# Kernel optimization log

Hardware: AMD Instinct MI355X
Metric: run time of the kernel (lower is better)

The kernel has to match this reference:

```python
import jax, jax.numpy as jnp
import numpy as np

B, C, H, W, G = 4, 256, 64, 64, 4
K = 9  # 3x3 kernel


def _conv1x1(x, w, b):
    return jnp.einsum('bchw,oc->bohw', x, w) + b[None, :, None, None]


def _deform_conv(V, offset, mask, weight, groups):
    # torchvision modulated deform_conv2d, stride=1, pad=1, dil=1, no bias.
    Bs, Cc, Hh, Ww = V.shape
    Cg = Cc // groups
    # offset layout: [B, og, K, 2(y,x), H, W]
    off = offset.reshape(Bs, groups, K, 2, Hh, Ww)
    ky, kx = jnp.meshgrid(jnp.arange(3), jnp.arange(3), indexing='ij')
    ky = ky.reshape(K).astype(offset.dtype)
    kx = kx.reshape(K).astype(offset.dtype)
    hh = jnp.arange(Hh, dtype=offset.dtype)
    ww = jnp.arange(Ww, dtype=offset.dtype)
    # sampling positions [B, G, K, H, W]
    py = off[:, :, :, 0] + (hh[:, None] - 1.0)[None, None, None] + ky[None, None, :, None, None]
    px = off[:, :, :, 1] + (ww[None, :] - 1.0)[None, None, None] + kx[None, None, :, None, None]
    y0f = jnp.floor(py)
    x0f = jnp.floor(px)
    fy = py - y0f
    fx = px - x0f
    y0 = y0f.astype(jnp.int32)
    x0 = x0f.astype(jnp.int32)
    Vg = V.reshape(Bs, groups, Cg, Hh * Ww)

    def gather(yi, xi, wgt):
        valid = (yi >= 0) & (yi < Hh) & (xi >= 0) & (xi < Ww)
        idx = (jnp.clip(yi, 0, Hh - 1) * Ww + jnp.clip(xi, 0, Ww - 1)).reshape(Bs, groups, 1, K * Hh * Ww)
        vals = jnp.take_along_axis(Vg, jnp.broadcast_to(idx, (Bs, groups, Cg, K * Hh * Ww)), axis=3)
        vals = vals.reshape(Bs, groups, Cg, K, Hh, Ww)
        return vals * (wgt * valid.astype(wgt.dtype))[:, :, None]

    sampled = (gather(y0, x0, (1.0 - fy) * (1.0 - fx))
               + gather(y0, x0 + 1, (1.0 - fy) * fx)
               + gather(y0 + 1, x0, fy * (1.0 - fx))
               + gather(y0 + 1, x0 + 1, fy * fx))  # [B, G, Cg, K, H, W]
    m = mask.reshape(Bs, groups, K, Hh, Ww)
    wk = weight.reshape(groups, Cc // groups, Cg, K)
    out = jnp.einsum('bgikhw,bgkhw,goik->bgohw', sampled, m, wk)
    return out.reshape(Bs, Cc, Hh, Ww)


def setup_inputs() -> dict:
    key = jax.random.key(0)
    ks = jax.random.split(key, 12)
    inp = {
        'rife_feat': jax.random.normal(ks[0], (B, C, H, W), jnp.float32),
        'd0': jax.random.normal(ks[1], (B, C, H, W), jnp.float32),
        'd1': jax.random.normal(ks[2], (B, C, H, W), jnp.float32),
        'wq': jax.random.normal(ks[3], (C, C), jnp.float32) * (1.0 / np.sqrt(C)),
        'bq': jax.random.normal(ks[4], (C,), jnp.float32) * 0.01,
        'wk': jax.random.normal(ks[5], (C, C), jnp.float32) * (1.0 / np.sqrt(C)),
        'bk': jax.random.normal(ks[6], (C,), jnp.float32) * 0.01,
        'wv': jax.random.normal(ks[7], (C, C), jnp.float32) * (1.0 / np.sqrt(C)),
        'bv': jax.random.normal(ks[8], (C,), jnp.float32) * 0.01,
        'w_off': jax.random.normal(ks[9], (27 * G, 2 * C, 3, 3), jnp.float32) * 0.02,
        'b_off': jnp.zeros((27 * G,), jnp.float32),
        'dcn_w': jax.random.normal(ks[10], (C, C // G, 3, 3), jnp.float32) * 0.05,
        'gamma': jnp.ones((1,), jnp.float32),
    }
    return inp


def reference(rife_feat, d0, d1, wq, bq, wk, bk, wv, bv, w_off, b_off, dcn_w, gamma):
    Qs = jnp.concatenate([rife_feat, rife_feat], axis=0)  # [2B, C, H, W]
    Ds = jnp.concatenate([d0, d1], axis=0)
    Q = _conv1x1(Qs, wq, bq)
    Kf = _conv1x1(Ds, wk, bk)
    V = _conv1x1(Ds, wv, bv)
    comb = jnp.concatenate([Q, Kf], axis=1)  # [2B, 2C, H, W]
    out = jax.lax.conv_general_dilated(comb, w_off, (1, 1), [(1, 1), (1, 1)],
                                       dimension_numbers=('NCHW', 'OIHW', 'NCHW'))
    out = out + b_off[None, :, None, None]  # [2B, 27G, H, W]
    n = out.shape[1] // 3
    o1, o2, mlog = out[:, :n], out[:, n:2 * n], out[:, 2 * n:]
    offset = jnp.concatenate([o1, o2], axis=1)  # [2B, 18G, H, W]
    mask = jax.nn.sigmoid(mlog)
    aligned = _deform_conv(V, offset, mask, dcn_w, G)
    a0, a1 = aligned[:B], aligned[B:]
    fused = rife_feat + gamma * (a0 + a1)
    return fused, offset[:B], offset[B:]
```

## Files before the change

### kernel.cpp

```cpp
#include <hip/hip_runtime.h>
#include <math.h>

#define HW   4096
#define CDIM 256

typedef float f32x4  __attribute__((ext_vector_type(4)));
typedef short short8 __attribute__((ext_vector_type(8)));

#define FUSED_SZ (4ULL*256*HW)
#define OFF_SZ   (4ULL*72*HW)

static __device__ __forceinline__ unsigned short f2b(float f) {
    unsigned u = __float_as_uint(f);
    unsigned r = (u + 0x7fffu + ((u >> 16) & 1u)) >> 16;
    return (unsigned short)r;
}
static __device__ __forceinline__ float b2f(short h) {
    return __uint_as_float(((unsigned)(unsigned short)h) << 16);
}
static __device__ __forceinline__ unsigned pk_bf16(float a, float b) {
    unsigned r;
    asm("v_cvt_pk_bf16_f32 %0, %1, %2" : "=v"(r) : "v"(a), "v"(b));
    return r;
}
union U8 { unsigned u[4]; short8 s; };

__global__ __launch_bounds__(256) void wprep(const float* __restrict__ w_off,
                                             unsigned short* __restrict__ wT2)
{
    int idx = blockIdx.x * 256 + threadIdx.x;
    if (idx >= 9 * 128 * 512) return;
    int kk  = idx / (128 * 512);
    int rem = idx - kk * 128 * 512;
    int o = rem >> 9;
    int c = rem & 511;
    float v = (o < 108) ? w_off[((size_t)o * 512 + c) * 9 + kk] : 0.f;
    size_t flat = ((size_t)(kk * 16 + (c >> 5)) * 128 + o) * 32 + (c & 31);
    wT2[flat] = f2b(v);
}

__global__ __launch_bounds__(256) void dprep(const float* __restrict__ dcn_w,
                                             unsigned short* __restrict__ dcnwT)
{
    int idx = blockIdx.x * 256 + threadIdx.x;
    if (idx >= 9 * 256 * 64) return;
    int k   = idx / (256 * 64);
    int rem = idx - k * 256 * 64;
    int og = rem >> 6;
    int i  = rem & 63;
    int g = og >> 6, ol = og & 63;
    size_t flat = ((size_t)((k * 4 + g) * 2 + (i >> 5)) * 64 + ol) * 32 + (i & 31);
    dcnwT[flat] = f2b(dcn_w[((size_t)og * 64 + i) * 9 + k]);
}

__global__ __launch_bounds__(256) void qwprep(
    const float* __restrict__ wq, const float* __restrict__ wk,
    const float* __restrict__ wv, unsigned short* __restrict__ wqkvT)
{
    int idx = blockIdx.x * 256 + threadIdx.x;
    int o = idx >> 8;
    int c = idx & 255;
    float v = (o < 256) ? wq[(size_t)o * 256 + c]
            : (o < 512) ? wk[(size_t)(o - 256) * 256 + c]
                        : wv[(size_t)(o - 512) * 256 + c];
    wqkvT[idx] = f2b(v);
}

__global__ __launch_bounds__(256) void xprep(
    const float* __restrict__ rife, const float* __restrict__ d0,
    const float* __restrict__ d1, unsigned short* __restrict__ xT)
{
    const int pix0 = blockIdx.x * 64;
    const int img  = blockIdx.y;
    const int t    = threadIdx.x;

    const float* src = (img < 4) ? rife + (size_t)img * CDIM * HW
                     : (img < 8) ? d0 + (size_t)(img - 4) * CDIM * HW
                                 : d1 + (size_t)(img - 8) * CDIM * HW;
    unsigned short* dst = xT + (size_t)img * 4096 * 256;

    __shared__ float tile[64][65];

    for (int c0 = 0; c0 < 256; c0 += 64) {
        #pragma unroll
        for (int r = 0; r < 16; ++r) {
            int idx = t + r * 256;
            int c = idx >> 6, pp = idx & 63;
            tile[c][pp] = src[(size_t)(c0 + c) * HW + pix0 + pp];
        }
        __syncthreads();
        const int pix = t >> 2, cq = t & 3;
        const int cb = cq * 16;
        uint4 p0, p1;
        p0.x = (unsigned)f2b(tile[cb+0][pix])  | ((unsigned)f2b(tile[cb+1][pix])  << 16);
        p0.y = (unsigned)f2b(tile[cb+2][pix])  | ((unsigned)f2b(tile[cb+3][pix])  << 16);
        p0.z = (unsigned)f2b(tile[cb+4][pix])  | ((unsigned)f2b(tile[cb+5][pix])  << 16);
        p0.w = (unsigned)f2b(tile[cb+6][pix])  | ((unsigned)f2b(tile[cb+7][pix])  << 16);
        p1.x = (unsigned)f2b(tile[cb+8][pix])  | ((unsigned)f2b(tile[cb+9][pix])  << 16);
        p1.y = (unsigned)f2b(tile[cb+10][pix]) | ((unsigned)f2b(tile[cb+11][pix]) << 16);
        p1.z = (unsigned)f2b(tile[cb+12][pix]) | ((unsigned)f2b(tile[cb+13][pix]) << 16);
        p1.w = (unsigned)f2b(tile[cb+14][pix]) | ((unsigned)f2b(tile[cb+15][pix]) << 16);
        unsigned short* p = dst + (size_t)(pix0 + pix) * 256 + c0 + cb;
        *(uint4*)p = p0;
        *(uint4*)(p + 8) = p1;
        __syncthreads();
    }
}

__global__ __launch_bounds__(256) void qkv_mfma(
    const unsigned short* __restrict__ xT,
    const unsigned short* __restrict__ wqkvT,
    const float* __restrict__ bq, const float* __restrict__ bk,
    const float* __restrict__ bv,
    unsigned short* __restrict__ comb_t, unsigned short* __restrict__ vbuf_t)
{
    const int pix0 = blockIdx.x * 64;
    const int type = blockIdx.y;
    const int s    = blockIdx.z;
    const int t    = threadIdx.x;
    const int wvi  = t >> 6;
    const int lane = t & 63;
    const int q    = lane >> 4;
    const int rl   = lane & 15;

    const int img = (type == 0) ? (s & 3) : (4 + s);
    const short8* X = (const short8*)(xT + (size_t)img * 4096 * 256);
    const short8* W = (const short8*)(wqkvT + (size_t)(type * 256 + wvi * 64) * 256);
    const float* bias = (type == 0) ? bq : (type == 1) ? bk : bv;

    f32x4 acc[4][4];
    #pragma unroll
    for (int mf = 0; mf < 4; ++mf)
        #pragma unroll
        for (int nf = 0; nf < 4; ++nf)
            acc[mf][nf] = (f32x4){0.f, 0.f, 0.f, 0.f};

    #pragma unroll
    for (int c8 = 0; c8 < 32; c8 += 4) {
        short8 a[4], b[4];
        #pragma unroll
        for (int mf = 0; mf < 4; ++mf)
            a[mf] = W[(size_t)(mf * 16 + rl) * 32 + c8 + q];
        #pragma unroll
        for (int nf = 0; nf < 4; ++nf)
            b[nf] = X[(size_t)(pix0 + nf * 16 + rl) * 32 + c8 + q];
        #pragma unroll
        for (int mf = 0; mf < 4; ++mf)
            #pragma unroll
            for (int nf = 0; nf < 4; ++nf)
                acc[mf][nf] = __builtin_amdgcn_mfma_f32_16x16x32_bf16(a[mf], b[nf], acc[mf][nf], 0, 0, 0);
    }

    const int CH = (type < 2) ? 512 : 256;
    unsigned short* dst = (type < 2)
        ? comb_t + (size_t)s * 4096 * 512 + type * 256
        : vbuf_t + (size_t)s * 4096 * 256;
    #pragma unroll
    for (int mf = 0; mf < 4; ++mf) {
        const int o_loc = wvi * 64 + mf * 16 + q * 4;
        const float4 bz = *(const float4*)(bias + o_loc);
        #pragma unroll
        for (int nf = 0; nf < 4; ++nf) {
            const int pix = pix0 + nf * 16 + rl;
            uint2 pk;
            pk.x = pk_bf16(acc[mf][nf][0] + bz.x, acc[mf][nf][1] + bz.y);
            pk.y = pk_bf16(acc[mf][nf][2] + bz.z, acc[mf][nf][3] + bz.w);
            *(uint2*)(dst + (size_t)pix * CH + o_loc) = pk;
        }
    }
}

__global__ __launch_bounds__(256) void offconv_mfma(
    const unsigned short* __restrict__ comb_t,
    const unsigned short* __restrict__ wT2,
    const float* __restrict__ b_off,
    float* __restrict__ dout, float* __restrict__ mask_ws)
{
    const int bid = blockIdx.x;
    const int s = bid & 7;
    const int h = bid >> 3;
    const int t = threadIdx.x;
    const int lane = t & 63;
    const int wid  = t >> 6;
    const int q    = lane >> 4;
    const int rl   = lane & 15;

    __shared__ __align__(16) unsigned short tb[2][792 * 8];

    const short8* cbv = (const short8*)comb_t + (size_t)s * 4096 * 64;
    const short8* wv  = (const short8*)wT2;

    const int i1 = t + 256, i2 = t + 512, i3 = t + 768;

    auto sload = [&](int idx, int c8) -> short8 {
        int x = idx >> 2, cq = idx & 3;
        int ky = x / 66, xx = x - ky * 66;
        int hh = h + ky - 1, gx = xx - 1;
        short8 v = {0, 0, 0, 0, 0, 0, 0, 0};
        if (hh >= 0 && hh < 64 && gx >= 0 && gx < 64)
            v = cbv[(size_t)(hh * 64 + gx) * 64 + c8 + cq];
        return v;
    };
    auto swrite = [&](unsigned short* buf, int idx, short8 v) {
        int x = idx >> 2, cq = idx & 3;
        int qs = cq ^ ((x >> 1) & 3);
        *((short8*)buf + x * 4 + qs) = v;
    };

    f32x4 acc[2][4];
    #pragma unroll
    for (int ma = 0; ma < 2; ++ma)
        #pragma unroll
        for (int nf = 0; nf < 4; ++nf)
            acc[ma][nf] = (f32x4){0.f, 0.f, 0.f, 0.f};

    short8 r0 = sload(t, 0), r1 = sload(i1, 0), r2 = sload(i2, 0);
    short8 r3 = {0,0,0,0,0,0,0,0};
    if (i3 < 792) r3 = sload(i3, 0);
    swrite(tb[0], t, r0); swrite(tb[0], i1, r1); swrite(tb[0], i2, r2);
    if (i3 < 792) swrite(tb[0], i3, r3);
    __syncthreads();

    for (int sl = 0; sl < 16; ++sl) {
        const int c8 = sl * 4;
        if (sl < 15) {
            r0 = sload(t, c8 + 4); r1 = sload(i1, c8 + 4); r2 = sload(i2, c8 + 4);
            if (i3 < 792) r3 = sload(i3, c8 + 4);
        }
        short8 a[2][9];
        #pragma unroll
        for (int ma = 0; ma < 2; ++ma) {
            const int o = (wid * 2 + ma) * 16 + rl;
            #pragma unroll
            for (int kk = 0; kk < 9; ++kk)
                a[ma][kk] = wv[((size_t)(kk * 16 + sl) * 128 + o) * 4 + q];
        }
        const unsigned short* bufc = tb[sl & 1];
        #pragma unroll
        for (int kk = 0; kk < 9; ++kk) {
            const int ky = kk / 3, kx = kk % 3;
            #pragma unroll
            for (int nf = 0; nf < 4; ++nf) {
                const int xr = ky * 66 + nf * 16 + rl + kx;
                short8 b = *((const short8*)bufc + xr * 4 + (q ^ ((xr >> 1) & 3)));
                acc[0][nf] = __builtin_amdgcn_mfma_f32_16x16x32_bf16(a[0][kk], b, acc[0][nf], 0, 0, 0);
                acc[1][nf] = __builtin_amdgcn_mfma_f32_16x16x32_bf16(a[1][kk], b, acc[1][nf], 0, 0, 0);
            }
        }
        if (sl < 15) {
            unsigned short* bufn = tb[(sl + 1) & 1];
            swrite(bufn, t, r0); swrite(bufn, i1, r1); swrite(bufn, i2, r2);
            if (i3 < 792) swrite(bufn, i3, r3);
        }
        __syncthreads();
    }

    const size_t obase = FUSED_SZ + (s < 4 ? 0 : OFF_SZ) + (size_t)(s & 3) * 72 * HW + (size_t)h * 64;
    const size_t mbase = (size_t)s * 36 * HW + (size_t)h * 64;
    #pragma unroll
    for (int ma = 0; ma < 2; ++ma) {
        #pragma unroll
        for (int r = 0; r < 4; ++r) {
            const int o = (wid * 2 + ma) * 16 + q * 4 + r;
            if (o >= 108) continue;
            const float bz = b_off[o];
            #pragma unroll
            for (int nf = 0; nf < 4; ++nf) {
                const int w = nf * 16 + rl;
                float v = acc[ma][nf][r] + bz;
                if (o < 72)
                    dout[obase + (size_t)o * HW + w] = v;
                else
                    mask_ws[mbase + (size_t)(o - 72) * HW + w] = 1.f / (1.f + expf(-v));
            }
        }
    }
}

__global__ __launch_bounds__(256) void dcn_fuse_mfma(
    const float* __restrict__ rife, const unsigned short* __restrict__ dcnwT,
    const float* __restrict__ gamma,
    const unsigned short* __restrict__ vbuf_t, const float* __restrict__ mask_ws,
    float* __restrict__ dout)
{
    const int bid = blockIdx.x;
    const int c   = bid & 15;
    const int h   = bid >> 4;
    const int b   = c >> 2;
    const int g   = c & 3;
    const int t    = threadIdx.x;
    const int wv   = t >> 6;
    const int lane = t & 63;
    const int q    = lane >> 4;
    const int rl   = lane & 15;
    const int pix  = wv * 16 + rl;

    const short8* aT = (const short8*)dcnwT;

    f32x4 acc[4];
    #pragma unroll
    for (int ma = 0; ma < 4; ++ma) acc[ma] = (f32x4){0.f, 0.f, 0.f, 0.f};

    const size_t obA = FUSED_SZ + (size_t)b * 72 * HW + (size_t)(g * 18) * HW + (size_t)h * 64 + pix;
    const size_t obB = obA + OFF_SZ;
    const size_t mbA = (size_t)b * 36 * HW + (size_t)(g * 9) * HW + (size_t)h * 64 + pix;
    const size_t mbB = mbA + 4ULL * 36 * HW;

    auto body = [&](float pyv, float pxv, float mv, int sb, short8 (&af)[4][2]) {
        const float y0f = floorf(pyv), x0f = floorf(pxv);
        const float fy = pyv - y0f, fx = pxv - x0f;
        const int y0 = (int)y0f, x0 = (int)x0f;
        const bool vy0 = (y0 >= 0) && (y0 < 64);
        const bool vy1 = (y0 >= -1) && (y0 < 63);
        const bool vx0 = (x0 >= 0) && (x0 < 64);
        const bool vx1 = (x0 >= -1) && (x0 < 63);
        const float w00 = (1.f - fy) * (1.f - fx) * mv * (float)(vy0 && vx0);
        const float w01 = (1.f - fy) * fx        * mv * (float)(vy0 && vx1);
        const float w10 = fy * (1.f - fx)        * mv * (float)(vy1 && vx0);
        const float w11 = fy * fx                * mv * (float)(vy1 && vx1);
        const int yc0 = min(max(y0, 0), 63),     yc1 = min(max(y0 + 1, 0), 63);
        const int xc0 = min(max(x0, 0), 63),     xc1 = min(max(x0 + 1, 0), 63);
        const size_t o00 = (size_t)(yc0 * 64 + xc0) * 256;
        const size_t o01 = (size_t)(yc0 * 64 + xc1) * 256;
        const size_t o10 = (size_t)(yc1 * 64 + xc0) * 256;
        const size_t o11 = (size_t)(yc1 * 64 + xc1) * 256;

        const unsigned short* Vb = vbuf_t + (size_t)sb * 4096 * 256 + g * 64 + q * 8;

        short8 v00a = *(const short8*)(Vb + o00);
        short8 v01a = *(const short8*)(Vb + o01);
        short8 v10a = *(const short8*)(Vb + o10);
        short8 v11a = *(const short8*)(Vb + o11);
        short8 v00b = *(const short8*)(Vb + o00 + 32);
        short8 v01b = *(const short8*)(Vb + o01 + 32);
        short8 v10b = *(const short8*)(Vb + o10 + 32);
        short8 v11b = *(const short8*)(Vb + o11 + 32);

        U8 u0, u1;
        #pragma unroll
        for (int j = 0; j < 4; ++j) {
            const int ce = 2 * j, co = 2 * j + 1;
            float e0 = w00 * b2f(v00a[ce]) + w01 * b2f(v01a[ce])
                     + w10 * b2f(v10a[ce]) + w11 * b2f(v11a[ce]);
            float e1 = w00 * b2f(v00a[co]) + w01 * b2f(v01a[co])
                     + w10 * b2f(v10a[co]) + w11 * b2f(v11a[co]);
            u0.u[j] = pk_bf16(e0, e1);
            float f0 = w00 * b2f(v00b[ce]) + w01 * b2f(v01b[ce])
                     + w10 * b2f(v10b[ce]) + w11 * b2f(v11b[ce]);
            float f1 = w00 * b2f(v00b[co]) + w01 * b2f(v01b[co])
                     + w10 * b2f(v10b[co]) + w11 * b2f(v11b[co]);
            u1.u[j] = pk_bf16(f0, f1);
        }
        short8 bf0 = u0.s, bf1 = u1.s;
        acc[0] = __builtin_amdgcn_mfma_f32_16x16x32_bf16(af[0][0], bf0, acc[0], 0, 0, 0);
        acc[1] = __builtin_amdgcn_mfma_f32_16x16x32_bf16(af[1][0], bf0, acc[1], 0, 0, 0);
        acc[2] = __builtin_amdgcn_mfma_f32_16x16x32_bf16(af[2][0], bf0, acc[2], 0, 0, 0);
        acc[3] = __builtin_amdgcn_mfma_f32_16x16x32_bf16(af[3][0], bf0, acc[3], 0, 0, 0);
        acc[0] = __builtin_amdgcn_mfma_f32_16x16x32_bf16(af[0][1], bf1, acc[0], 0, 0, 0);
        acc[1] = __builtin_amdgcn_mfma_f32_16x16x32_bf16(af[1][1], bf1, acc[1], 0, 0, 0);
        acc[2] = __builtin_amdgcn_mfma_f32_16x16x32_bf16(af[2][1], bf1, acc[2], 0, 0, 0);
        acc[3] = __builtin_amdgcn_mfma_f32_16x16x32_bf16(af[3][1], bf1, acc[3], 0, 0, 0);
    };

    float cyA = dout[obA],      cxA = dout[obA + HW],      cmA = mask_ws[mbA];
    float cyB = dout[obB],      cxB = dout[obB + HW],      cmB = mask_ws[mbB];

    #pragma unroll
    for (int k = 0; k < 9; ++k) {
        const int ky = k / 3, kx = k % 3;
        short8 af[4][2];
        #pragma unroll
        for (int ma = 0; ma < 4; ++ma)
            #pragma unroll
            for (int ks = 0; ks < 2; ++ks)
                af[ma][ks] = aT[((size_t)((k * 4 + g) * 2 + ks) * 64 + ma * 16 + rl) * 4 + q];
        float nyA = 0.f, nxA = 0.f, nmA = 0.f, nyB = 0.f, nxB = 0.f, nmB = 0.f;
        if (k < 8) {
            nyA = dout[obA + (size_t)((k + 1) * 2) * HW];
            nxA = dout[obA + (size_t)((k + 1) * 2 + 1) * HW];
            nmA = mask_ws[mbA + (size_t)(k + 1) * HW];
            nyB = dout[obB + (size_t)((k + 1) * 2) * HW];
            nxB = dout[obB + (size_t)((k + 1) * 2 + 1) * HW];
            nmB = mask_ws[mbB + (size_t)(k + 1) * HW];
        }
        body(cyA + (float)(h - 1 + ky), cxA + (float)(pix - 1 + kx), cmA, b,     af);
        body(cyB + (float)(h - 1 + ky), cxB + (float)(pix - 1 + kx), cmB, b + 4, af);
        if (k < 8) { cyA = nyA; cxA = nxA; cmA = nmA; cyB = nyB; cxB = nxB; cmB = nmB; }
    }

    const float gm = gamma[0];
    #pragma unroll
    for (int ma = 0; ma < 4; ++ma) {
        #pragma unroll
        for (int r = 0; r < 4; ++r) {
            const int o = g * 64 + ma * 16 + q * 4 + r;
            const size_t addr = ((size_t)b * 256 + o) * HW + (size_t)h * 64 + pix;
            dout[addr] = rife[addr] + gm * acc[ma][r];
        }
    }
}

extern "C" void kernel_launch(void* const* d_in, const int* in_sizes, int n_in,
                              void* d_out, int out_size, void* d_ws, size_t ws_size,
                              hipStream_t stream)
{
    const float* rife  = (const float*)d_in[0];
    const float* d0    = (const float*)d_in[1];
    const float* d1    = (const float*)d_in[2];
    const float* wq    = (const float*)d_in[3];
    const float* bq    = (const float*)d_in[4];
    const float* wk    = (const float*)d_in[5];
    const float* bk    = (const float*)d_in[6];
    const float* wv    = (const float*)d_in[7];
    const float* bv    = (const float*)d_in[8];
    const float* w_off = (const float*)d_in[9];
    const float* b_off = (const float*)d_in[10];
    const float* dcnw  = (const float*)d_in[11];
    const float* gamma = (const float*)d_in[12];
    float* out = (float*)d_out;
    char* wsb  = (char*)d_ws;

    unsigned short* comb_t = (unsigned short*)(wsb);
    unsigned short* vbuf_t = (unsigned short*)(wsb + 33554432);
    float*          mws    = (float*)(wsb + 50331648);
    unsigned short* wT2    = (unsigned short*)(wsb + 55050240);
    unsigned short* dcnwT  = (unsigned short*)(wsb + 56229888);
    unsigned short* xT     = (unsigned short*)(wsb + 56524800);
    unsigned short* wqkvT  = (unsigned short*)(wsb + 81690624);

    wprep<<<2304, 256, 0, stream>>>(w_off, wT2);
    dprep<<<576, 256, 0, stream>>>(dcnw, dcnwT);
    qwprep<<<768, 256, 0, stream>>>(wq, wk, wv, wqkvT);
    xprep<<<dim3(64, 12), 256, 0, stream>>>(rife, d0, d1, xT);
    qkv_mfma<<<dim3(64, 3, 8), 256, 0, stream>>>(xT, wqkvT, bq, bk, bv, comb_t, vbuf_t);
    offconv_mfma<<<512, 256, 0, stream>>>(comb_t, wT2, b_off, out, mws);
    dcn_fuse_mfma<<<1024, 256, 0, stream>>>(rife, dcnwT, gamma, vbuf_t, mws, out);
}
```

Baseline: 215.6 us.

## Merge weight-prep kernels, use packed bf16 convert, restructure DCN gather loop

Three weight-preparation kernels are merged into one launch with block-range dispatch, removing two kernel launches. The xprep transpose now uses the hardware packed bf16 convert instead of manual rounding. The deformable-conv loop is restructured to compute bilinear weights up front, then per 32-channel half load the A weights and both images' corner samples and issue the MFMAs. The k-loop is no longer force-unrolled, which may reduce register pressure but could lose scheduling freedom.

```diff
diff --git a/kernel.cpp b/kernel.cpp
--- a/kernel.cpp
+++ b/kernel.cpp
@@ -25,45 +25,43 @@
 }
 union U8 { unsigned u[4]; short8 s; };
 
-__global__ __launch_bounds__(256) void wprep(const float* __restrict__ w_off,
-                                             unsigned short* __restrict__ wT2)
-{
-    int idx = blockIdx.x * 256 + threadIdx.x;
-    if (idx >= 9 * 128 * 512) return;
-    int kk  = idx / (128 * 512);
-    int rem = idx - kk * 128 * 512;
-    int o = rem >> 9;
-    int c = rem & 511;
-    float v = (o < 108) ? w_off[((size_t)o * 512 + c) * 9 + kk] : 0.f;
-    size_t flat = ((size_t)(kk * 16 + (c >> 5)) * 128 + o) * 32 + (c & 31);
-    wT2[flat] = f2b(v);
-}
-
-__global__ __launch_bounds__(256) void dprep(const float* __restrict__ dcn_w,
-                                             unsigned short* __restrict__ dcnwT)
-{
-    int idx = blockIdx.x * 256 + threadIdx.x;
-    if (idx >= 9 * 256 * 64) return;
-    int k   = idx / (256 * 64);
-    int rem = idx - k * 256 * 64;
-    int og = rem >> 6;
-    int i  = rem & 63;
-    int g = og >> 6, ol = og & 63;
-    size_t flat = ((size_t)((k * 4 + g) * 2 + (i >> 5)) * 64 + ol) * 32 + (i & 31);
-    dcnwT[flat] = f2b(dcn_w[((size_t)og * 64 + i) * 9 + k]);
-}
-
-__global__ __launch_bounds__(256) void qwprep(
+__global__ __launch_bounds__(256) void prep_all(
+    const float* __restrict__ w_off, const float* __restrict__ dcn_w,
     const float* __restrict__ wq, const float* __restrict__ wk,
-    const float* __restrict__ wv, unsigned short* __restrict__ wqkvT)
-{
-    int idx = blockIdx.x * 256 + threadIdx.x;
-    int o = idx >> 8;
-    int c = idx & 255;
-    float v = (o < 256) ? wq[(size_t)o * 256 + c]
-            : (o < 512) ? wk[(size_t)(o - 256) * 256 + c]
-                        : wv[(size_t)(o - 512) * 256 + c];
-    wqkvT[idx] = f2b(v);
+    const float* __restrict__ wv,
+    unsigned short* __restrict__ wT2, unsigned short* __restrict__ dcnwT,
+    unsigned short* __restrict__ wqkvT)
+{
+    const int bid = blockIdx.x;
+    if (bid < 2304) {
+        int idx = bid * 256 + threadIdx.x;
+        int kk  = idx / (128 * 512);
+        int rem = idx - kk * 128 * 512;
+        int o = rem >> 9;
+        int c = rem & 511;
+        float v = (o < 108) ? w_off[((size_t)o * 512 + c) * 9 + kk] : 0.f;
+        size_t flat = ((size_t)(kk * 16 + (c >> 5)) * 128 + o) * 32 + (c & 31);
+        wT2[flat] = f2b(v);
+    } else if (bid < 2880) {
+        int idx = (bid - 2304) * 256 + threadIdx.x;
+        if (idx < 9 * 256 * 64) {
+            int k   = idx / (256 * 64);
+            int rem = idx - k * 256 * 64;
+            int og = rem >> 6;
+            int i  = rem & 63;
+            int g = og >> 6, ol = og & 63;
+            size_t flat = ((size_t)((k * 4 + g) * 2 + (i >> 5)) * 64 + ol) * 32 + (i & 31);
+            dcnwT[flat] = f2b(dcn_w[((size_t)og * 64 + i) * 9 + k]);
+        }
+    } else {
+        int idx = (bid - 2880) * 256 + threadIdx.x;
+        int o = idx >> 8;
+        int c = idx & 255;
+        float v = (o < 256) ? wq[(size_t)o * 256 + c]
+                : (o < 512) ? wk[(size_t)(o - 256) * 256 + c]
+                            : wv[(size_t)(o - 512) * 256 + c];
+        wqkvT[idx] = f2b(v);
+    }
 }
 
 __global__ __launch_bounds__(256) void xprep(
@@ -92,14 +90,14 @@
         const int pix = t >> 2, cq = t & 3;
         const int cb = cq * 16;
         uint4 p0, p1;
-        p0.x = (unsigned)f2b(tile[cb+0][pix])  | ((unsigned)f2b(tile[cb+1][pix])  << 16);
-        p0.y = (unsigned)f2b(tile[cb+2][pix])  | ((unsigned)f2b(tile[cb+3][pix])  << 16);
-        p0.z = (unsigned)f2b(tile[cb+4][pix])  | ((unsigned)f2b(tile[cb+5][pix])  << 16);
-        p0.w = (unsigned)f2b(tile[cb+6][pix])  | ((unsigned)f2b(tile[cb+7][pix])  << 16);
-        p1.x = (unsigned)f2b(tile[cb+8][pix])  | ((unsigned)f2b(tile[cb+9][pix])  << 16);
-        p1.y = (unsigned)f2b(tile[cb+10][pix]) | ((unsigned)f2b(tile[cb+11][pix]) << 16);
-        p1.z = (unsigned)f2b(tile[cb+12][pix]) | ((unsigned)f2b(tile[cb+13][pix]) << 16);
-        p1.w = (unsigned)f2b(tile[cb+14][pix]) | ((unsigned)f2b(tile[cb+15][pix]) << 16);
+        p0.x = pk_bf16(tile[cb+0][pix],  tile[cb+1][pix]);
+        p0.y = pk_bf16(tile[cb+2][pix],  tile[cb+3][pix]);
+        p0.z = pk_bf16(tile[cb+4][pix],  tile[cb+5][pix]);
+        p0.w = pk_bf16(tile[cb+6][pix],  tile[cb+7][pix]);
+        p1.x = pk_bf16(tile[cb+8][pix],  tile[cb+9][pix]);
+        p1.y = pk_bf16(tile[cb+10][pix], tile[cb+11][pix]);
+        p1.z = pk_bf16(tile[cb+12][pix], tile[cb+13][pix]);
+        p1.w = pk_bf16(tile[cb+14][pix], tile[cb+15][pix]);
         unsigned short* p = dst + (size_t)(pix0 + pix) * 256 + c0 + cb;
         *(uint4*)p = p0;
         *(uint4*)(p + 8) = p1;
@@ -306,75 +304,60 @@
     const size_t mbA = (size_t)b * 36 * HW + (size_t)(g * 9) * HW + (size_t)h * 64 + pix;
     const size_t mbB = mbA + 4ULL * 36 * HW;
 
-    auto body = [&](float pyv, float pxv, float mv, int sb, short8 (&af)[4][2]) {
-        const float y0f = floorf(pyv), x0f = floorf(pxv);
-        const float fy = pyv - y0f, fx = pxv - x0f;
+    const unsigned short* VbA = vbuf_t + (size_t)b * 4096 * 256 + g * 64 + q * 8;
+    const unsigned short* VbB = VbA + 4ULL * 4096 * 256;
+
+    auto bil = [&](float py, float px, float mv,
+                   float& w00, float& w01, float& w10, float& w11,
+                   size_t& o00, size_t& o01, size_t& o10, size_t& o11) {
+        const float y0f = floorf(py), x0f = floorf(px);
+        const float fy = py - y0f, fx = px - x0f;
         const int y0 = (int)y0f, x0 = (int)x0f;
         const bool vy0 = (y0 >= 0) && (y0 < 64);
         const bool vy1 = (y0 >= -1) && (y0 < 63);
         const bool vx0 = (x0 >= 0) && (x0 < 64);
         const bool vx1 = (x0 >= -1) && (x0 < 63);
-        const float w00 = (1.f - fy) * (1.f - fx) * mv * (float)(vy0 && vx0);
-        const float w01 = (1.f - fy) * fx        * mv * (float)(vy0 && vx1);
-        const float w10 = fy * (1.f - fx)        * mv * (float)(vy1 && vx0);
-        const float w11 = fy * fx                * mv * (float)(vy1 && vx1);
+        w00 = (1.f - fy) * (1.f - fx) * mv * (float)(vy0 && vx0);
+        w01 = (1.f - fy) * fx        * mv * (float)(vy0 && vx1);
+        w10 = fy * (1.f - fx)        * mv * (float)(vy1 && vx0);
+        w11 = fy * fx                * mv * (float)(vy1 && vx1);
         const int yc0 = min(max(y0, 0), 63),     yc1 = min(max(y0 + 1, 0), 63);
         const int xc0 = min(max(x0, 0), 63),     xc1 = min(max(x0 + 1, 0), 63);
-        const size_t o00 = (size_t)(yc0 * 64 + xc0) * 256;
-        const size_t o01 = (size_t)(yc0 * 64 + xc1) * 256;
-        const size_t o10 = (size_t)(yc1 * 64 + xc0) * 256;
-        const size_t o11 = (size_t)(yc1 * 64 + xc1) * 256;
-
-        const unsigned short* Vb = vbuf_t + (size_t)sb * 4096 * 256 + g * 64 + q * 8;
-
-        short8 v00a = *(const short8*)(Vb + o00);
-        short8 v01a = *(const short8*)(Vb + o01);
-        short8 v10a = *(const short8*)(Vb + o10);
-        short8 v11a = *(const short8*)(Vb + o11);
-        short8 v00b = *(const short8*)(Vb + o00 + 32);
-        short8 v01b = *(const short8*)(Vb + o01 + 32);
-        short8 v10b = *(const short8*)(Vb + o10 + 32);
-        short8 v11b = *(const short8*)(Vb + o11 + 32);
-
-        U8 u0, u1;
+        o00 = (size_t)(yc0 * 64 + xc0) * 256;
+        o01 = (size_t)(yc0 * 64 + xc1) * 256;
+        o10 = (size_t)(yc1 * 64 + xc0) * 256;
+        o11 = (size_t)(yc1 * 64 + xc1) * 256;
+    };
+    auto blend1 = [&](short8 c00, short8 c01, short8 c10, short8 c11,
+                      float w00, float w01, float w10, float w11) -> short8 {
+        U8 u;
         #pragma unroll
         for (int j = 0; j < 4; ++j) {
             const int ce = 2 * j, co = 2 * j + 1;
-            float e0 = w00 * b2f(v00a[ce]) + w01 * b2f(v01a[ce])
-                     + w10 * b2f(v10a[ce]) + w11 * b2f(v11a[ce]);
-            float e1 = w00 * b2f(v00a[co]) + w01 * b2f(v01a[co])
-                     + w10 * b2f(v10a[co]) + w11 * b2f(v11a[co]);
-            u0.u[j] = pk_bf16(e0, e1);
-            float f0 = w00 * b2f(v00b[ce]) + w01 * b2f(v01b[ce])
-                     + w10 * b2f(v10b[ce]) + w11 * b2f(v11b[ce]);
-            float f1 = w00 * b2f(v00b[co]) + w01 * b2f(v01b[co])
-                     + w10 * b2f(v10b[co]) + w11 * b2f(v11b[co]);
-            u1.u[j] = pk_bf16(f0, f1);
-        }
-        short8 bf0 = u0.s, bf1 = u1.s;
-        acc[0] = __builtin_amdgcn_mfma_f32_16x16x32_bf16(af[0][0], bf0, acc[0], 0, 0, 0);
-        acc[1] = __builtin_amdgcn_mfma_f32_16x16x32_bf16(af[1][0], bf0, acc[1], 0, 0, 0);
-        acc[2] = __builtin_amdgcn_mfma_f32_16x16x32_bf16(af[2][0], bf0, acc[2], 0, 0, 0);
-        acc[3] = __builtin_amdgcn_mfma_f32_16x16x32_bf16(af[3][0], bf0, acc[3], 0, 0, 0);
-        acc[0] = __builtin_amdgcn_mfma_f32_16x16x32_bf16(af[0][1], bf1, acc[0], 0, 0, 0);
-        acc[1] = __builtin_amdgcn_mfma_f32_16x16x32_bf16(af[1][1], bf1, acc[1], 0, 0, 0);
-        acc[2] = __builtin_amdgcn_mfma_f32_16x16x32_bf16(af[2][1], bf1, acc[2], 0, 0, 0);
-        acc[3] = __builtin_amdgcn_mfma_f32_16x16x32_bf16(af[3][1], bf1, acc[3], 0, 0, 0);
+            float e0 = w00 * b2f(c00[ce]) + w01 * b2f(c01[ce])
+                     + w10 * b2f(c10[ce]) + w11 * b2f(c11[ce]);
+            float e1 = w00 * b2f(c00[co]) + w01 * b2f(c01[co])
+                     + w10 * b2f(c10[co]) + w11 * b2f(c11[co]);
+            u.u[j] = pk_bf16(e0, e1);
+        }
+        return u.s;
     };
 
-    float cyA = dout[obA],      cxA = dout[obA + HW],      cmA = mask_ws[mbA];
-    float cyB = dout[obB],      cxB = dout[obB + HW],      cmB = mask_ws[mbB];
-
-    #pragma unroll
+    float cyA = dout[obA], cxA = dout[obA + HW], cmA = mask_ws[mbA];
+    float cyB = dout[obB], cxB = dout[obB + HW], cmB = mask_ws[mbB];
+
     for (int k = 0; k < 9; ++k) {
-        const int ky = k / 3, kx = k % 3;
-        short8 af[4][2];
-        #pragma unroll
-        for (int ma = 0; ma < 4; ++ma)
-            #pragma unroll
-            for (int ks = 0; ks < 2; ++ks)
-                af[ma][ks] = aT[((size_t)((k * 4 + g) * 2 + ks) * 64 + ma * 16 + rl) * 4 + q];
-        float nyA = 0.f, nxA = 0.f, nmA = 0.f, nyB = 0.f, nxB = 0.f, nmB = 0.f;
+        const int ky = k / 3, kx = k - ky * 3;
+
+        float wA00, wA01, wA10, wA11, wB00, wB01, wB10, wB11;
+        size_t oA00, oA01, oA10, oA11, oB00, oB01, oB10, oB11;
+        bil(cyA + (float)(h - 1 + ky), cxA + (float)(pix - 1 + kx), cmA,
+            wA00, wA01, wA10, wA11, oA00, oA01, oA10, oA11);
+        bil(cyB + (float)(h - 1 + ky), cxB + (float)(pix - 1 + kx), cmB,
+            wB00, wB01, wB10, wB11, oB00, oB01, oB10, oB11);
+
+        float nyA = cyA, nxA = cxA, nmA = cmA;
+        float nyB = cyB, nxB = cxB, nmB = cmB;
         if (k < 8) {
             nyA = dout[obA + (size_t)((k + 1) * 2) * HW];
             nxA = dout[obA + (size_t)((k + 1) * 2 + 1) * HW];
@@ -383,9 +366,37 @@
             nxB = dout[obB + (size_t)((k + 1) * 2 + 1) * HW];
             nmB = mask_ws[mbB + (size_t)(k + 1) * HW];
         }
-        body(cyA + (float)(h - 1 + ky), cxA + (float)(pix - 1 + kx), cmA, b,     af);
-        body(cyB + (float)(h - 1 + ky), cxB + (float)(pix - 1 + kx), cmB, b + 4, af);
-        if (k < 8) { cyA = nyA; cxA = nxA; cmA = nmA; cyB = nyB; cxB = nxB; cmB = nmB; }
+
+        #pragma unroll
+        for (int ks = 0; ks < 2; ++ks) {
+            const int co = ks * 32;
+            short8 af0 = aT[((size_t)((k * 4 + g) * 2 + ks) * 64 + 0 * 16 + rl) * 4 + q];
+            short8 af1 = aT[((size_t)((k * 4 + g) * 2 + ks) * 64 + 1 * 16 + rl) * 4 + q];
+            short8 af2 = aT[((size_t)((k * 4 + g) * 2 + ks) * 64 + 2 * 16 + rl) * 4 + q];
+            short8 af3 = aT[((size_t)((k * 4 + g) * 2 + ks) * 64 + 3 * 16 + rl) * 4 + q];
+            short8 A00 = *(const short8*)(VbA + oA00 + co);
+            short8 A01 = *(const short8*)(VbA + oA01 + co);
+            short8 A10 = *(const short8*)(VbA + oA10 + co);
+            short8 A11 = *(const short8*)(VbA + oA11 + co);
+            short8 B00 = *(const short8*)(VbB + oB00 + co);
+            short8 B01 = *(const short8*)(VbB + oB01 + co);
+            short8 B10 = *(const short8*)(VbB + oB10 + co);
+            short8 B11 = *(const short8*)(VbB + oB11 + co);
+
+            short8 bfA = blend1(A00, A01, A10, A11, wA00, wA01, wA10, wA11);
+            acc[0] = __builtin_amdgcn_mfma_f32_16x16x32_bf16(af0, bfA, acc[0], 0, 0, 0);
+            acc[1] = __builtin_amdgcn_mfma_f32_16x16x32_bf16(af1, bfA, acc[1], 0, 0, 0);
+            acc[2] = __builtin_amdgcn_mfma_f32_16x16x32_bf16(af2, bfA, acc[2], 0, 0, 0);
+            acc[3] = __builtin_amdgcn_mfma_f32_16x16x32_bf16(af3, bfA, acc[3], 0, 0, 0);
+            short8 bfB = blend1(B00, B01, B10, B11, wB00, wB01, wB10, wB11);
+            acc[0] = __builtin_amdgcn_mfma_f32_16x16x32_bf16(af0, bfB, acc[0], 0, 0, 0);
+            acc[1] = __builtin_amdgcn_mfma_f32_16x16x32_bf16(af1, bfB, acc[1], 0, 0, 0);
+            acc[2] = __builtin_amdgcn_mfma_f32_16x16x32_bf16(af2, bfB, acc[2], 0, 0, 0);
+            acc[3] = __builtin_amdgcn_mfma_f32_16x16x32_bf16(af3, bfB, acc[3], 0, 0, 0);
+        }
+
+        cyA = nyA; cxA = nxA; cmA = nmA;
+        cyB = nyB; cxB = nxB; cmB = nmB;
     }
 
     const float gm = gamma[0];
@@ -428,9 +439,7 @@
     unsigned short* xT     = (unsigned short*)(wsb + 56524800);
     unsigned short* wqkvT  = (unsigned short*)(wsb + 81690624);
 
-    wprep<<<2304, 256, 0, stream>>>(w_off, wT2);
-    dprep<<<576, 256, 0, stream>>>(dcnw, dcnwT);
-    qwprep<<<768, 256, 0, stream>>>(wq, wk, wv, wqkvT);
+    prep_all<<<3648, 256, 0, stream>>>(w_off, dcnw, wq, wk, wv, wT2, dcnwT, wqkvT);
     xprep<<<dim3(64, 12), 256, 0, stream>>>(rife, d0, d1, xT);
     qkv_mfma<<<dim3(64, 3, 8), 256, 0, stream>>>(xT, wqkvT, bq, bk, bv, comb_t, vbuf_t);
     offconv_mfma<<<512, 256, 0, stream>>>(comb_t, wT2, b_off, out, mws);
```

Result: slower. 220.0 us (+2.1%).
